# Kernel tuning notes

Measured on AMD Instinct MI355X. Metric: run time of the kernel, lower is better.

## Reference

```python
import jax, jax.numpy as jnp
import numpy as np

B, S, A, H, N = 4096, 128, 32, 1024, 256
BETA = 1.0            # params['temperature']
NORM_SMOOTHING = 0.01 # params['norm_smoothing']
MAX_A = 1.0           # env.action_space.high[0]
# dropout_rate = 0.0 and eval-mode reference -> dropout is identity


def setup_inputs() -> dict:
    key = jax.random.key(0)
    ks = jax.random.split(key, 16)
    sc_s = 1.0 / np.sqrt(S)
    sc_h = 1.0 / np.sqrt(H)
    return {
        "s": jax.random.normal(ks[0], (B, S), jnp.float32),
        "a": jax.random.normal(ks[1], (B, A), jnp.float32),
        # value side MLP: S->H->H->H->N
        "Wv1": jax.random.uniform(ks[2], (S, H), jnp.float32, -sc_s, sc_s),
        "bv1": jax.random.uniform(ks[3], (H,), jnp.float32, -sc_s, sc_s),
        "Wv2": jax.random.uniform(ks[4], (H, H), jnp.float32, -sc_h, sc_h),
        "bv2": jax.random.uniform(ks[5], (H,), jnp.float32, -sc_h, sc_h),
        "Wv3": jax.random.uniform(ks[6], (H, H), jnp.float32, -sc_h, sc_h),
        "bv3": jax.random.uniform(ks[7], (H,), jnp.float32, -sc_h, sc_h),
        "Wv4": jax.random.uniform(ks[8], (H, N), jnp.float32, -sc_h, sc_h),
        "bv4": jax.random.uniform(ks[9], (N,), jnp.float32, -sc_h, sc_h),
        # location side: S->H (xavier), then N expert linears H->A stacked
        "Wl1": jax.random.normal(ks[10], (S, H), jnp.float32) * np.sqrt(2.0 / (S + H)),
        "bl1": jnp.zeros((H,), jnp.float32),
        "Wexp": jax.random.uniform(ks[11], (N, H, A), jnp.float32, -0.1, 0.1),
        "bexp": jax.random.uniform(ks[12], (N, A), jnp.float32, -1.0, 1.0),
    }


def reference(s, a, Wv1, bv1, Wv2, bv2, Wv3, bv3, Wv4, bv4, Wl1, bl1, Wexp, bexp):
    t = jax.nn.relu(s @ Wv1 + bv1)
    t = jax.nn.relu(t @ Wv2 + bv2)
    t = jax.nn.relu(t @ Wv3 + bv3)
    values = t @ Wv4 + bv4                      # [B, N]

    # --- get_all_centroids: shared hidden, N expert heads as grouped GEMM ---
    h = jax.nn.relu(s @ Wl1 + bl1)              # [B, H] (dropout identity)
    centroids = MAX_A * jnp.tanh(
        jnp.einsum("bh,nha->bna", h, Wexp) + bexp[None]
    )                                           # [B, N, A]

    # --- rbf_function: softmax over -beta * ||centroid - a|| ---
    diff = centroids - a[:, None, :]            # [B, N, A]
    dist = jnp.sqrt(jnp.sum(diff * diff, axis=2) + NORM_SMOOTHING)  # [B, N]
    weights = jax.nn.softmax(-BETA * dist, axis=1)                  # [B, N]

    return jnp.sum(weights * values, axis=1, keepdims=True)         # [B, 1]
```

## Files before the change

kernel.cpp:

```cpp
#include <hip/hip_runtime.h>
#include <hip/hip_bf16.h>


typedef _Float16 half8 __attribute__((ext_vector_type(8)));
typedef _Float16 half4v __attribute__((ext_vector_type(4)));
typedef float floatx16 __attribute__((ext_vector_type(16)));

namespace {
constexpr int kB = 4096, kS = 128, kA = 32, kH = 1024, kN = 256;
constexpr size_t al(size_t x) { return (x + 255) & ~size_t(255); }
constexpr size_t OFF_FLAG  = 0;
constexpr size_t OFF_S16   = 256;
constexpr size_t OFF_WEXPT = OFF_S16   + al((size_t)kB * kS * 2);
constexpr size_t OFF_BUF2  = OFF_WEXPT + al((size_t)kN * kA * kH * 2);
constexpr size_t OFF_VAL   = OFF_BUF2  + al((size_t)kB * kH * 2);
constexpr size_t OFF_WV1T  = OFF_VAL   + al((size_t)kB * kN * 4);
constexpr size_t OFF_WV2T  = OFF_WV1T  + al((size_t)kS * kH * 2);
constexpr size_t OFF_WV3T  = OFF_WV2T  + al((size_t)kH * kH * 2);
constexpr size_t OFF_WV4T  = OFF_WV3T  + al((size_t)kH * kH * 2);
constexpr size_t OFF_WL1T  = OFF_WV4T  + al((size_t)kH * kN * 2);
constexpr size_t OFF_BUF1  = OFF_WL1T  + al((size_t)kS * kH * 2);
constexpr size_t OFF_Z     = OFF_WV1T;
}

__device__ __forceinline__ float ldraw(const void* p, size_t i, int bf) {
    if (bf) return __uint_as_float(((unsigned)((const unsigned short*)p)[i]) << 16);
    return ((const float*)p)[i];
}

__device__ __forceinline__ float4 ldraw4(const void* p, size_t i, int bf) {
    if (bf) {
        ushort4 u = *(const ushort4*)((const unsigned short*)p + i);
        return make_float4(__uint_as_float((unsigned)u.x << 16),
                           __uint_as_float((unsigned)u.y << 16),
                           __uint_as_float((unsigned)u.z << 16),
                           __uint_as_float((unsigned)u.w << 16));
    }
    return *(const float4*)((const float*)p + i);
}

__device__ __forceinline__ void gl_lds16(const _Float16* g, _Float16* l) {
    __builtin_amdgcn_global_load_lds(
        (const __attribute__((address_space(1))) unsigned int*)g,
        (__attribute__((address_space(3))) unsigned int*)l, 16, 0, 0);
}

__device__ __forceinline__ float fast_tanh(float x) {
    x = fminf(9.f, fmaxf(-9.f, x));
    float e = __expf(2.f * x);
    return (e - 1.f) * __builtin_amdgcn_rcpf(e + 1.f);
}

__global__ void detect_kernel(const unsigned int* __restrict__ s_raw, int* __restrict__ flag) {
    __shared__ int cnt;
    if (threadIdx.x == 0) cnt = 0;
    __syncthreads();
    const unsigned e = (s_raw[threadIdx.x] >> 7) & 0xFFu;
    int c = (e >= 118u && e <= 135u) ? 1 : 0;
    for (int off = 32; off > 0; off >>= 1) c += __shfl_down(c, off);
    if ((threadIdx.x & 63) == 0) atomicAdd(&cnt, c);
    __syncthreads();
    if (threadIdx.x == 0) *flag = (cnt > 128) ? 1 : 0;
}

__global__ void convert_to_f16(const void* __restrict__ src, _Float16* __restrict__ dst,
                               int n, const int* __restrict__ flag) {
    const int bf = *flag;
    int i = blockIdx.x * blockDim.x + threadIdx.x;
    const int stride = gridDim.x * blockDim.x;
    for (; i < n; i += stride) dst[i] = (_Float16)ldraw(src, i, bf);
}

struct TDesc { const void* src; _Float16* dst; int K; int N; int tiles; };
struct TPack { TDesc d[6]; };

__global__ void transpose_all(TPack p, const int* __restrict__ flag) {
    __shared__ float tile[32][33];
    const int bf = *flag;
    int bid = blockIdx.x;
    int i = 0;
    while (bid >= p.d[i].tiles) { bid -= p.d[i].tiles; ++i; }
    const int K = p.d[i].K, N = p.d[i].N;
    const int tpz = (N >> 5) * (K >> 5);
    const int z = bid / tpz, r = bid - z * tpz;
    const int n0 = (r % (N >> 5)) * 32, k0 = (r / (N >> 5)) * 32;
    const size_t zo = (size_t)z * K * N;
    const void* src = p.d[i].src;
    _Float16* dst = p.d[i].dst;
    const int tx = threadIdx.x, ty = threadIdx.y;
    float4 v = ldraw4(src, zo + (size_t)(k0 + ty) * N + n0 + tx * 4, bf);
    tile[ty][tx * 4 + 0] = v.x;
    tile[ty][tx * 4 + 1] = v.y;
    tile[ty][tx * 4 + 2] = v.z;
    tile[ty][tx * 4 + 3] = v.w;
    __syncthreads();
    half4v o;
#pragma unroll
    for (int j = 0; j < 4; ++j) o[j] = (_Float16)tile[tx * 4 + j][ty];
    *(half4v*)(dst + zo + (size_t)(n0 + ty) * K + k0 + tx * 4) = o;
}

template <int TM, int TN, int WM, int WN, int DO_RELU, int OUT_F16>
__launch_bounds__(WM * WN * 64, 2)
__global__ void dgemm(const _Float16* __restrict__ A, const _Float16* __restrict__ Bt,
                      const void* __restrict__ bias_raw, void* __restrict__ Cout,
                      const int* __restrict__ flagp, int N, int K, int Mt, int Nt) {
    constexpr int NT = WM * WN * 64;
    constexpr int BK = 32;
    constexpr int MI = TM / WM / 32, NI = TN / WN / 32;
    constexpr int ACH = TM * BK / 8;
    constexpr int BCH = TN * BK / 8;
    constexpr int AT = (ACH + NT - 1) / NT;
    constexpr int BT = (BCH + NT - 1) / NT;
    __shared__ _Float16 As[2 * ACH * 8];
    __shared__ _Float16 Bs[2 * BCH * 8];

    const int tid = threadIdx.x;
    const int lane = tid & 63;
    const int w = tid >> 6, wr = w / WN, wc = w % WN;

    int mt, nt;
    {
        const int bid = blockIdx.x;
        if ((Mt & 7) == 0 && (Nt & 7) == 0) {
            const int xcd = bid & 7, loc = bid >> 3;
            const int Bn = Nt >> 3;
            const int sr = loc / (8 * Bn);
            const int rem = loc - sr * (8 * Bn);
            mt = sr * 8 + (rem & 7);
            nt = xcd * Bn + (rem >> 3);
        } else {
            mt = bid % Mt;
            nt = bid / Mt;
        }
    }
    const int m0 = mt * TM, n0 = nt * TN;

    const _Float16* gAsrc[AT];
    _Float16* lAdst[AT];
#pragma unroll
    for (int t = 0; t < AT; ++t) {
        int c = t * NT + tid;
        if (c >= ACH) c = ACH - 1;
        const int ks = c / (TM * 2), rem = c % (TM * 2);
        const int row = (rem >> 6) * 32 + (rem & 31);
        const int kcol = ks * 16 + ((rem >> 5) & 1) * 8;
        gAsrc[t] = A + (size_t)(m0 + row) * K + kcol;
        lAdst[t] = As + c * 8;
    }
    const _Float16* gBsrc[BT];
    _Float16* lBdst[BT];
#pragma unroll
    for (int t = 0; t < BT; ++t) {
        int c = t * NT + tid;
        if (c >= BCH) c = BCH - 1;
        const int ks = c / (TN * 2), rem = c % (TN * 2);
        const int row = (rem >> 6) * 32 + (rem & 31);
        const int kcol = ks * 16 + ((rem >> 5) & 1) * 8;
        gBsrc[t] = Bt + (size_t)(n0 + row) * K + kcol;
        lBdst[t] = Bs + c * 8;
    }

    auto issue = [&](int k0, int st) {
#pragma unroll
        for (int t = 0; t < AT; ++t)
            if ((t + 1) * NT <= ACH || t * NT + tid < ACH)
                gl_lds16(gAsrc[t] + k0, lAdst[t] + st * ACH * 8);
#pragma unroll
        for (int t = 0; t < BT; ++t)
            if ((t + 1) * NT <= BCH || t * NT + tid < BCH)
                gl_lds16(gBsrc[t] + k0, lBdst[t] + st * BCH * 8);
    };

    floatx16 acc[MI][NI];
#pragma unroll
    for (int mi = 0; mi < MI; ++mi)
#pragma unroll
        for (int ni = 0; ni < NI; ++ni)
#pragma unroll
            for (int i = 0; i < 16; ++i) acc[mi][ni][i] = 0.f;

    auto compute = [&](int st) {
#pragma unroll
        for (int ks = 0; ks < 2; ++ks) {
            half8 af[MI], bf[NI];
#pragma unroll
            for (int mi = 0; mi < MI; ++mi)
                af[mi] = *(const half8*)(As + st * ACH * 8 + ((size_t)(ks * TM * 2 + (wr * MI + mi) * 64 + lane)) * 8);
#pragma unroll
            for (int ni = 0; ni < NI; ++ni)
                bf[ni] = *(const half8*)(Bs + st * BCH * 8 + ((size_t)(ks * TN * 2 + (wc * NI + ni) * 64 + lane)) * 8);
#pragma unroll
            for (int mi = 0; mi < MI; ++mi)
#pragma unroll
                for (int ni = 0; ni < NI; ++ni)
                    acc[mi][ni] = __builtin_amdgcn_mfma_f32_32x32x16_f16(af[mi], bf[ni], acc[mi][ni], 0, 0, 0);
        }
    };

    issue(0, 0);
    for (int k0 = 0; k0 < K; k0 += 2 * BK) {
        __syncthreads();
        if (k0 + BK < K) issue(k0 + BK, 1);
        compute(0);
        __syncthreads();
        if (k0 + 2 * BK < K) issue(k0 + 2 * BK, 0);
        compute(1);
    }

    const int bf_ = *flagp;
    const int am = lane & 31;
    const int half = lane >> 5;
#pragma unroll
    for (int mi = 0; mi < MI; ++mi)
#pragma unroll
        for (int ni = 0; ni < NI; ++ni) {
            const int Rb = m0 + (wr * MI + mi) * 32;
            const int Cb = n0 + (wc * NI + ni) * 32 + am;
            const float bv = ldraw(bias_raw, Cb, bf_);
#pragma unroll
            for (int rr = 0; rr < 16; ++rr) {
                const int row = Rb + (rr & 3) + 8 * (rr >> 2) + 4 * half;
                float x = acc[mi][ni][rr] + bv;
                if (DO_RELU) x = fmaxf(x, 0.f);
                if (OUT_F16) ((_Float16*)Cout)[(size_t)row * N + Cb] = (_Float16)x;
                else ((float*)Cout)[(size_t)row * N + Cb] = x;
            }
        }
}

__launch_bounds__(256)
__global__ void final_fused(const _Float16* __restrict__ z, const void* __restrict__ a_raw,
                            const float* __restrict__ values, const int* __restrict__ flag,
                            void* __restrict__ out) {
    const int b = blockIdx.x;
    const int n = threadIdx.x;
    const int bf = *flag;
    __shared__ float as_[32];
    if (n < 32) as_[n] = ldraw(a_raw, (size_t)b * kA + n, bf);
    __syncthreads();

    const _Float16* zp = z + (size_t)b * (kN * kA) + n * kA;
    float zl[32];
#pragma unroll
    for (int t = 0; t < 4; ++t) {
        half8 h = *(const half8*)(zp + t * 8);
#pragma unroll
        for (int j = 0; j < 8; ++j) zl[t * 8 + j] = (float)h[j];
    }
    float sum = 0.f;
#pragma unroll
    for (int a = 0; a < 32; ++a) {
        const float c = fast_tanh(zl[a]);
        const float d = c - as_[a];
        sum = fmaf(d, d, sum);
    }
    const float dist = sqrtf(sum + 0.01f);
    const float v = values[(size_t)b * kN + n];

    const int wid = n >> 6, lane = n & 63;
    __shared__ float red[8];
    __shared__ float rw[4], rwv[4];
    float m = dist;
    for (int off = 32; off > 0; off >>= 1) m = fminf(m, __shfl_down(m, off));
    if (lane == 0) red[wid] = m;
    __syncthreads();
    if (n == 0) red[4] = fminf(fminf(red[0], red[1]), fminf(red[2], red[3]));
    __syncthreads();
    const float dmin = red[4];

    float wgt = expf(dmin - dist);
    float wv = wgt * v;
    for (int off = 32; off > 0; off >>= 1) {
        wgt += __shfl_down(wgt, off);
        wv += __shfl_down(wv, off);
    }
    if (lane == 0) { rw[wid] = wgt; rwv[wid] = wv; }
    __syncthreads();
    if (n == 0) {
        const float sw = rw[0] + rw[1] + rw[2] + rw[3];
        const float swv = rwv[0] + rwv[1] + rwv[2] + rwv[3];
        const float o = swv / sw;
        if (bf) ((__hip_bfloat16*)out)[b] = __float2bfloat16(o);
        else    ((float*)out)[b] = o;
    }
}

extern "C" void kernel_launch(void* const* d_in, const int* in_sizes, int n_in,
                              void* d_out, int out_size, void* d_ws, size_t ws_size,
                              hipStream_t stream) {
    (void)in_sizes; (void)n_in; (void)out_size; (void)ws_size;
    char* ws = (char*)d_ws;
    int* flag = (int*)(ws + OFF_FLAG);
    _Float16* s16   = (_Float16*)(ws + OFF_S16);
    _Float16* wv1t  = (_Float16*)(ws + OFF_WV1T);
    _Float16* wv2t  = (_Float16*)(ws + OFF_WV2T);
    _Float16* wv3t  = (_Float16*)(ws + OFF_WV3T);
    _Float16* wv4t  = (_Float16*)(ws + OFF_WV4T);
    _Float16* wl1t  = (_Float16*)(ws + OFF_WL1T);
    _Float16* wexpt = (_Float16*)(ws + OFF_WEXPT);
    _Float16* buf1  = (_Float16*)(ws + OFF_BUF1);
    _Float16* buf2  = (_Float16*)(ws + OFF_BUF2);
    float* values   = (float*)(ws + OFF_VAL);
    _Float16* z     = (_Float16*)(ws + OFF_Z);

    detect_kernel<<<1, 256, 0, stream>>>((const unsigned int*)d_in[0], flag);
    convert_to_f16<<<512, 256, 0, stream>>>(d_in[0], s16, kB * kS, flag);

    TPack tp;
    tp.d[0] = {d_in[2],  wv1t,  kS, kH, (kH / 32) * (kS / 32)};
    tp.d[1] = {d_in[4],  wv2t,  kH, kH, (kH / 32) * (kH / 32)};
    tp.d[2] = {d_in[6],  wv3t,  kH, kH, (kH / 32) * (kH / 32)};
    tp.d[3] = {d_in[8],  wv4t,  kH, kN, (kN / 32) * (kH / 32)};
    tp.d[4] = {d_in[10], wl1t,  kS, kH, (kH / 32) * (kS / 32)};
    tp.d[5] = {d_in[12], wexpt, kH, kA, kN * (kA / 32) * (kH / 32)};
    int total_tiles = 0;
    for (int i = 0; i < 6; ++i) total_tiles += tp.d[i].tiles;
    transpose_all<<<total_tiles, dim3(8, 32), 0, stream>>>(tp, flag);

    dgemm<64, 64, 2, 2, 1, 1><<<(kB / 64) * (kH / 64), 256, 0, stream>>>(s16,  wv1t, d_in[3], buf1, flag, kH, kS, kB / 64, kH / 64);
    dgemm<128, 128, 2, 2, 1, 1><<<(kB / 128) * (kH / 128), 256, 0, stream>>>(buf1, wv2t, d_in[5], buf2, flag, kH, kH, kB / 128, kH / 128);
    dgemm<128, 128, 2, 2, 1, 1><<<(kB / 128) * (kH / 128), 256, 0, stream>>>(buf2, wv3t, d_in[7], buf1, flag, kH, kH, kB / 128, kH / 128);
    dgemm<64, 64, 2, 2, 0, 0><<<(kB / 64) * (kN / 64), 256, 0, stream>>>(buf1, wv4t, d_in[9], values, flag, kN, kH, kB / 64, kN / 64);
    dgemm<64, 64, 2, 2, 1, 1><<<(kB / 64) * (kH / 64), 256, 0, stream>>>(s16,  wl1t, d_in[11], buf2, flag, kH, kS, kB / 64, kH / 64);
    dgemm<256, 256, 4, 4, 0, 1><<<(kB / 256) * ((kN * kA) / 256), 1024, 0, stream>>>(buf2, wexpt, d_in[13], z, flag, kN * kA, kH, kB / 256, (kN * kA) / 256);
    final_fused<<<kB, 256, 0, stream>>>(z, d_in[1], values, flag, d_out);
}
```

Before: 315.3 us.

## Merge first-layer GEMMs and co-schedule expert GEMM with value layer 2

Wv1 and Wl1 are placed next to each other in the workspace so both first-layer GEMMs that read s run as one GEMM with N=2H, using a split bias select. The large expert grouped GEMM and the second value-MLP GEMM are launched together in one dual kernel with 256x256 tiles, filling the GPU with both jobs at once. Layer-2 value now uses 256x256 tiles, giving only 64 blocks, and the GEMM template moves relu/output flags to runtime arguments. This cuts launch count and the tail idle time of serialized small GEMMs, at the cost of runtime branches in the epilogue and a coarser tile for the value layer.

Result: slower. 328.6 us (+4.2%).

```diff
diff --git a/kernel.cpp b/kernel.cpp
--- a/kernel.cpp
+++ b/kernel.cpp
@@ -12,15 +12,16 @@
 constexpr size_t OFF_FLAG  = 0;
 constexpr size_t OFF_S16   = 256;
 constexpr size_t OFF_WEXPT = OFF_S16   + al((size_t)kB * kS * 2);
-constexpr size_t OFF_BUF2  = OFF_WEXPT + al((size_t)kN * kA * kH * 2);
-constexpr size_t OFF_VAL   = OFF_BUF2  + al((size_t)kB * kH * 2);
-constexpr size_t OFF_WV1T  = OFF_VAL   + al((size_t)kB * kN * 4);
-constexpr size_t OFF_WV2T  = OFF_WV1T  + al((size_t)kS * kH * 2);
+constexpr size_t OFF_WV1T  = OFF_WEXPT + al((size_t)kN * kA * kH * 2);
+constexpr size_t OFF_WL1T  = OFF_WV1T  + (size_t)kS * kH * 2;
+constexpr size_t OFF_WV2T  = OFF_WL1T  + al((size_t)kS * kH * 2);
 constexpr size_t OFF_WV3T  = OFF_WV2T  + al((size_t)kH * kH * 2);
 constexpr size_t OFF_WV4T  = OFF_WV3T  + al((size_t)kH * kH * 2);
-constexpr size_t OFF_WL1T  = OFF_WV4T  + al((size_t)kH * kN * 2);
-constexpr size_t OFF_BUF1  = OFF_WL1T  + al((size_t)kS * kH * 2);
-constexpr size_t OFF_Z     = OFF_WV1T;
+constexpr size_t OFF_BUFC  = OFF_WV4T  + al((size_t)kH * kN * 2);
+constexpr size_t OFF_B2V   = OFF_BUFC  + al((size_t)kB * 2 * kH * 2);
+constexpr size_t OFF_B3    = OFF_B2V   + al((size_t)kB * kH * 2);
+constexpr size_t OFF_VAL   = OFF_B3    + al((size_t)kB * kH * 2);
+constexpr size_t OFF_Z     = OFF_VAL   + al((size_t)kB * kN * 4);
 }
 
 __device__ __forceinline__ float ldraw(const void* p, size_t i, int bf) {
@@ -100,11 +101,18 @@
     *(half4v*)(dst + zo + (size_t)(n0 + ty) * K + k0 + tx * 4) = o;
 }
 
-template <int TM, int TN, int WM, int WN, int DO_RELU, int OUT_F16>
-__launch_bounds__(WM * WN * 64, 2)
-__global__ void dgemm(const _Float16* __restrict__ A, const _Float16* __restrict__ Bt,
-                      const void* __restrict__ bias_raw, void* __restrict__ Cout,
-                      const int* __restrict__ flagp, int N, int K, int Mt, int Nt) {
+struct GArgs {
+    const _Float16* A;
+    const _Float16* Bt;
+    const void* bias;
+    const void* bias2;
+    void* C;
+    int split;
+    int N, K, lda, Mt, Nt, relu, of16;
+};
+
+template <int TM, int TN, int WM, int WN>
+__device__ __forceinline__ void dgemm_core(const GArgs& g, int bid, const int* flagp) {
     constexpr int NT = WM * WN * 64;
     constexpr int BK = 32;
     constexpr int MI = TM / WM / 32, NI = TN / WN / 32;
@@ -118,21 +126,19 @@
     const int tid = threadIdx.x;
     const int lane = tid & 63;
     const int w = tid >> 6, wr = w / WN, wc = w % WN;
+    const int N = g.N, K = g.K, lda = g.lda;
 
     int mt, nt;
-    {
-        const int bid = blockIdx.x;
-        if ((Mt & 7) == 0 && (Nt & 7) == 0) {
-            const int xcd = bid & 7, loc = bid >> 3;
-            const int Bn = Nt >> 3;
-            const int sr = loc / (8 * Bn);
-            const int rem = loc - sr * (8 * Bn);
-            mt = sr * 8 + (rem & 7);
-            nt = xcd * Bn + (rem >> 3);
-        } else {
-            mt = bid % Mt;
-            nt = bid / Mt;
-        }
+    if ((g.Mt & 7) == 0 && (g.Nt & 7) == 0) {
+        const int xcd = bid & 7, loc = bid >> 3;
+        const int Bn = g.Nt >> 3;
+        const int sr = loc / (8 * Bn);
+        const int rem = loc - sr * (8 * Bn);
+        mt = sr * 8 + (rem & 7);
+        nt = xcd * Bn + (rem >> 3);
+    } else {
+        mt = bid % g.Mt;
+        nt = bid / g.Mt;
     }
     const int m0 = mt * TM, n0 = nt * TN;
 
@@ -145,7 +151,7 @@
         const int ks = c / (TM * 2), rem = c % (TM * 2);
         const int row = (rem >> 6) * 32 + (rem & 31);
         const int kcol = ks * 16 + ((rem >> 5) & 1) * 8;
-        gAsrc[t] = A + (size_t)(m0 + row) * K + kcol;
+        gAsrc[t] = g.A + (size_t)(m0 + row) * lda + kcol;
         lAdst[t] = As + c * 8;
     }
     const _Float16* gBsrc[BT];
@@ -157,7 +163,7 @@
         const int ks = c / (TN * 2), rem = c % (TN * 2);
         const int row = (rem >> 6) * 32 + (rem & 31);
         const int kcol = ks * 16 + ((rem >> 5) & 1) * 8;
-        gBsrc[t] = Bt + (size_t)(n0 + row) * K + kcol;
+        gBsrc[t] = g.Bt + (size_t)(n0 + row) * K + kcol;
         lBdst[t] = Bs + c * 8;
     }
 
@@ -217,16 +223,31 @@
         for (int ni = 0; ni < NI; ++ni) {
             const int Rb = m0 + (wr * MI + mi) * 32;
             const int Cb = n0 + (wc * NI + ni) * 32 + am;
-            const float bv = ldraw(bias_raw, Cb, bf_);
+            const float bv = (Cb < g.split) ? ldraw(g.bias, Cb, bf_)
+                                            : ldraw(g.bias2, Cb - g.split, bf_);
 #pragma unroll
             for (int rr = 0; rr < 16; ++rr) {
                 const int row = Rb + (rr & 3) + 8 * (rr >> 2) + 4 * half;
                 float x = acc[mi][ni][rr] + bv;
-                if (DO_RELU) x = fmaxf(x, 0.f);
-                if (OUT_F16) ((_Float16*)Cout)[(size_t)row * N + Cb] = (_Float16)x;
-                else ((float*)Cout)[(size_t)row * N + Cb] = x;
+                if (g.relu) x = fmaxf(x, 0.f);
+                if (g.of16) ((_Float16*)g.C)[(size_t)row * N + Cb] = (_Float16)x;
+                else ((float*)g.C)[(size_t)row * N + Cb] = x;
             }
         }
+}
+
+template <int TM, int TN, int WM, int WN>
+__launch_bounds__(WM * WN * 64, 2)
+__global__ void dgemm_one(GArgs g, const int* __restrict__ flagp) {
+    dgemm_core<TM, TN, WM, WN>(g, blockIdx.x, flagp);
+}
+
+template <int TM, int TN, int WM, int WN>
+__launch_bounds__(WM * WN * 64, 2)
+__global__ void dgemm_dual(GArgs g0, GArgs g1, int nb0, const int* __restrict__ flagp) {
+    const int bid = blockIdx.x;
+    if (bid < nb0) dgemm_core<TM, TN, WM, WN>(g0, bid, flagp);
+    else           dgemm_core<TM, TN, WM, WN>(g1, bid - nb0, flagp);
 }
 
 __launch_bounds__(256)
@@ -293,14 +314,15 @@
     char* ws = (char*)d_ws;
     int* flag = (int*)(ws + OFF_FLAG);
     _Float16* s16   = (_Float16*)(ws + OFF_S16);
+    _Float16* wexpt = (_Float16*)(ws + OFF_WEXPT);
     _Float16* wv1t  = (_Float16*)(ws + OFF_WV1T);
+    _Float16* wl1t  = (_Float16*)(ws + OFF_WL1T);
     _Float16* wv2t  = (_Float16*)(ws + OFF_WV2T);
     _Float16* wv3t  = (_Float16*)(ws + OFF_WV3T);
     _Float16* wv4t  = (_Float16*)(ws + OFF_WV4T);
-    _Float16* wl1t  = (_Float16*)(ws + OFF_WL1T);
-    _Float16* wexpt = (_Float16*)(ws + OFF_WEXPT);
-    _Float16* buf1  = (_Float16*)(ws + OFF_BUF1);
-    _Float16* buf2  = (_Float16*)(ws + OFF_BUF2);
+    _Float16* bufC  = (_Float16*)(ws + OFF_BUFC);
+    _Float16* b2v   = (_Float16*)(ws + OFF_B2V);
+    _Float16* b3    = (_Float16*)(ws + OFF_B3);
     float* values   = (float*)(ws + OFF_VAL);
     _Float16* z     = (_Float16*)(ws + OFF_Z);
 
@@ -309,20 +331,39 @@
 
     TPack tp;
     tp.d[0] = {d_in[2],  wv1t,  kS, kH, (kH / 32) * (kS / 32)};
-    tp.d[1] = {d_in[4],  wv2t,  kH, kH, (kH / 32) * (kH / 32)};
-    tp.d[2] = {d_in[6],  wv3t,  kH, kH, (kH / 32) * (kH / 32)};
-    tp.d[3] = {d_in[8],  wv4t,  kH, kN, (kN / 32) * (kH / 32)};
-    tp.d[4] = {d_in[10], wl1t,  kS, kH, (kH / 32) * (kS / 32)};
+    tp.d[1] = {d_in[10], wl1t,  kS, kH, (kH / 32) * (kS / 32)};
+    tp.d[2] = {d_in[4],  wv2t,  kH, kH, (kH / 32) * (kH / 32)};
+    tp.d[3] = {d_in[6],  wv3t,  kH, kH, (kH / 32) * (kH / 32)};
+    tp.d[4] = {d_in[8],  wv4t,  kH, kN, (kN / 32) * (kH / 32)};
     tp.d[5] = {d_in[12], wexpt, kH, kA, kN * (kA / 32) * (kH / 32)};
     int total_tiles = 0;
     for (int i = 0; i < 6; ++i) total_tiles += tp.d[i].tiles;
     transpose_all<<<total_tiles, dim3(8, 32), 0, stream>>>(tp, flag);
 
-    dgemm<64, 64, 2, 2, 1, 1><<<(kB / 64) * (kH / 64), 256, 0, stream>>>(s16,  wv1t, d_in[3], buf1, flag, kH, kS, kB / 64, kH / 64);
-    dgemm<128, 128, 2, 2, 1, 1><<<(kB / 128) * (kH / 128), 256, 0, stream>>>(buf1, wv2t, d_in[5], buf2, flag, kH, kH, kB / 128, kH / 128);
-    dgemm<128, 128, 2, 2, 1, 1><<<(kB / 128) * (kH / 128), 256, 0, stream>>>(buf2, wv3t, d_in[7], buf1, flag, kH, kH, kB / 128, kH / 128);
-    dgemm<64, 64, 2, 2, 0, 0><<<(kB / 64) * (kN / 64), 256, 0, stream>>>(buf1, wv4t, d_in[9], values, flag, kN, kH, kB / 64, kN / 64);
-    dgemm<64, 64, 2, 2, 1, 1><<<(kB / 64) * (kH / 64), 256, 0, stream>>>(s16,  wl1t, d_in[11], buf2, flag, kH, kS, kB / 64, kH / 64);
-    dgemm<256, 256, 4, 4, 0, 1><<<(kB / 256) * ((kN * kA) / 256), 1024, 0, stream>>>(buf2, wexpt, d_in[13], z, flag, kN * kA, kH, kB / 256, (kN * kA) / 256);
+    const int BIG = 1 << 30;
+    {
+        GArgs g{s16, wv1t, d_in[3], d_in[11], bufC, kH,
+                2 * kH, kS, kS, kB / 64, (2 * kH) / 64, 1, 1};
+        dgemm_one<64, 64, 2, 2><<<(kB / 64) * ((2 * kH) / 64), 256, 0, stream>>>(g, flag);
+    }
+    {
+        GArgs ge{bufC + kH, wexpt, d_in[13], d_in[13], z, BIG,
+                 kN * kA, kH, 2 * kH, kB / 256, (kN * kA) / 256, 0, 1};
+        GArgs g2{bufC, wv2t, d_in[5], d_in[5], b2v, BIG,
+                 kH, kH, 2 * kH, kB / 256, kH / 256, 1, 1};
+        const int nb0 = (kB / 256) * ((kN * kA) / 256);
+        const int nb1 = (kB / 256) * (kH / 256);
+        dgemm_dual<256, 256, 4, 4><<<nb0 + nb1, 1024, 0, stream>>>(ge, g2, nb0, flag);
+    }
+    {
+        GArgs g{b2v, wv3t, d_in[7], d_in[7], b3, BIG,
+                kH, kH, kH, kB / 128, kH / 128, 1, 1};
+        dgemm_one<128, 128, 2, 2><<<(kB / 128) * (kH / 128), 256, 0, stream>>>(g, flag);
+    }
+    {
+        GArgs g{b3, wv4t, d_in[9], d_in[9], values, BIG,
+                kN, kH, kH, kB / 64, kN / 64, 0, 0};
+        dgemm_one<64, 64, 2, 2><<<(kB / 64) * (kN / 64), 256, 0, stream>>>(g, flag);
+    }
     final_fused<<<kB, 256, 0, stream>>>(z, d_in[1], values, flag, d_out);
 }
```
